# Optimization experiments

Measured on AMD Instinct MI355X. Metric: run time of the kernel, lower is better.

Reference implementation:

```python
import jax, jax.numpy as jnp
import numpy as np
import math

D_MODEL = 512
N_HEADS = 8
D_HEAD = D_MODEL // N_HEADS
B, T = 2, 2048


def quant_linear(x, W, b, bitwidth):
    # BitNet-b1.58 style: ternary weights (per-tensor absmean scale),
    # activations quantized to signed `bitwidth` with per-token absmax scale.
    ws = jnp.mean(jnp.abs(W)) + 1e-5
    Wq = jnp.clip(jnp.round(W / ws), -1.0, 1.0)
    Qb = 2.0 ** (bitwidth - 1) - 1.0
    xs = Qb / (jnp.max(jnp.abs(x), axis=-1, keepdims=True) + 1e-5)
    xq = jnp.clip(jnp.round(x * xs), -Qb, Qb)
    return (xq @ W.T if False else jnp.einsum('...i,oi->...o', xq, Wq)) * (ws / xs) + b


def layer_norm(x, g, b, eps=1e-5):
    mu = jnp.mean(x, axis=-1, keepdims=True)
    var = jnp.mean(jnp.square(x - mu), axis=-1, keepdims=True)
    return (x - mu) * jax.lax.rsqrt(var + eps) * g + b


def rel_shift(x):
    # x: [B, H, T, T]
    b, h, t1, t2 = x.shape
    x = jnp.pad(x, ((0, 0), (0, 0), (0, 0), (1, 0)))  # [B,H,T,T+1]
    x = x.reshape(b, h, t2 + 1, t1)[:, :, 1:, :]
    return x.reshape(b, h, t1, t2)


def setup_inputs() -> dict:
    key = jax.random.key(0)
    ks = jax.random.split(key, 16)
    s = 0.02
    inp = {
        'x': jax.random.normal(ks[0], (B, T, D_MODEL), jnp.float32),
        'mask': jnp.ones((B, T, T), jnp.int32),
        'pos_emb': jax.random.normal(ks[1], (1, T, D_MODEL), jnp.float32),
        'ln_g': jnp.ones((D_MODEL,), jnp.float32),
        'ln_b': jnp.zeros((D_MODEL,), jnp.float32),
        'Wq': jax.random.normal(ks[2], (D_MODEL, D_MODEL), jnp.float32) * s,
        'bq': jnp.zeros((D_MODEL,), jnp.float32),
        'Wk': jax.random.normal(ks[3], (D_MODEL, D_MODEL), jnp.float32) * s,
        'bk': jnp.zeros((D_MODEL,), jnp.float32),
        'Wv': jax.random.normal(ks[4], (D_MODEL, D_MODEL), jnp.float32) * s,
        'bv': jnp.zeros((D_MODEL,), jnp.float32),
        'Wp': jax.random.normal(ks[5], (D_MODEL, D_MODEL), jnp.float32) * s,
        'bp': jnp.zeros((D_MODEL,), jnp.float32),
        'Wo': jax.random.normal(ks[6], (D_MODEL, D_MODEL), jnp.float32) * s,
        'bo': jnp.zeros((D_MODEL,), jnp.float32),
        'pos_bias_u': jax.random.normal(ks[7], (N_HEADS, D_HEAD), jnp.float32) * 0.01,
        'pos_bias_v': jax.random.normal(ks[8], (N_HEADS, D_HEAD), jnp.float32) * 0.01,
        'bitwidth': 8,
    }
    return inp


def reference(x, mask, pos_emb, ln_g, ln_b, Wq, bq, Wk, bk, Wv, bv, Wp, bp, Wo, bo, pos_bias_u, pos_bias_v, bitwidth):
    b, t, c = x.shape
    y = layer_norm(x, ln_g, ln_b)
    # projections -> [B, H, T, Dh]
    Q = quant_linear(y, Wq, bq, bitwidth).reshape(b, t, N_HEADS, D_HEAD).transpose(0, 2, 1, 3)
    K = quant_linear(y, Wk, bk, bitwidth).reshape(b, t, N_HEADS, D_HEAD).transpose(0, 2, 1, 3)
    V = quant_linear(y, Wv, bv, bitwidth).reshape(b, t, N_HEADS, D_HEAD).transpose(0, 2, 1, 3)
    p = quant_linear(pos_emb, Wp, bp, bitwidth).reshape(1, t, N_HEADS, D_HEAD).transpose(0, 2, 1, 3)
    Qu = Q + pos_bias_u[None, :, None, :]
    Qv = Q + pos_bias_v[None, :, None, :]
    matrix_ac = jnp.einsum('bhqd,bhkd->bhqk', Qu, K)
    matrix_bd = rel_shift(jnp.einsum('bhqd,xhkd->bhqk', Qv, p))
    scores = (matrix_ac + matrix_bd) / math.sqrt(D_HEAD)
    scores = jnp.where(mask[:, None, :, :] == 0, -jnp.inf, scores)
    A = jnp.nan_to_num(jax.nn.softmax(scores, axis=-1), nan=0.0)
    H = jnp.einsum('bhqk,bhkd->bhqd', A, V).transpose(0, 2, 1, 3).reshape(b, t, c)
    H = quant_linear(H, Wo, bo, bitwidth)
    H = H * mask[:, :, 0:1].astype(H.dtype)  # seq mask
    return x + H
```

## Files before the change

kernel.cpp:

```cpp
#include <hip/hip_runtime.h>
#include <math.h>

#define TT 2048
#define DMODEL 512
#define NHEADS 8
#define DHEAD 64
#define NBATCH 2
#define MTOK (NBATCH*TT)
#define NSPLIT 4
#define SC 0.18033688011112042f
#define PADQ 68

typedef unsigned short u16;
typedef unsigned int u32;
typedef __bf16 bf16x8 __attribute__((ext_vector_type(8)));
typedef float f32x4 __attribute__((ext_vector_type(4)));
typedef short s16x4 __attribute__((ext_vector_type(4)));
typedef short s16x8 __attribute__((ext_vector_type(8)));
typedef unsigned short u16x4 __attribute__((ext_vector_type(4)));
typedef int s32x4 __attribute__((ext_vector_type(4)));

#define MFMA16(a,b,c) __builtin_amdgcn_mfma_f32_16x16x32_bf16(a,b,c,0,0,0)
#define MFMA_PV(a,b,c) __builtin_amdgcn_mfma_f32_16x16x16bf16_1k(a,b,c,0,0,0)

__device__ __forceinline__ u16 f2b(float f){
  u32 x = __float_as_uint(f);
  x = x + 0x7fffu + ((x >> 16) & 1u);
  return (u16)(x >> 16);
}
__device__ __forceinline__ float b2f(u16 u){
  return __uint_as_float(((u32)u) << 16);
}
__device__ __forceinline__ u32 cvtpk(float lo, float hi){
  u32 d; asm("v_cvt_pk_bf16_f32 %0, %1, %2" : "=v"(d) : "v"(lo), "v"(hi)); return d;
}
__device__ __forceinline__ size_t fidx(int t, int d){
  return ((size_t)((t>>4)*16 + (d>>5)))*512
       + (size_t)(((((d>>3)&3)*16) + (t&15))*8 + (d&7));
}

__global__ __launch_bounds__(256) void wprep1_kernel(
    const float* __restrict__ W0, const float* __restrict__ W1,
    const float* __restrict__ W2, const float* __restrict__ W3,
    const float* __restrict__ W4, float* __restrict__ partial)
{
  int widx = blockIdx.y;
  const float* W = (widx==0)?W0:(widx==1)?W1:(widx==2)?W2:(widx==3)?W3:W4;
  size_t base = (size_t)blockIdx.x * 4096;
  int tid = threadIdx.x;
  float s = 0.f;
  for (int i = tid; i < 4096; i += 256) s += fabsf(W[base + i]);
  __shared__ float red[256];
  red[tid] = s; __syncthreads();
  for (int o = 128; o > 0; o >>= 1){ if (tid < o) red[tid] += red[tid+o]; __syncthreads(); }
  if (tid == 0) partial[widx*64 + blockIdx.x] = red[0];
}

__global__ __launch_bounds__(256) void wprep2_kernel(
    const float* __restrict__ W0, const float* __restrict__ W1,
    const float* __restrict__ W2, const float* __restrict__ W3,
    const float* __restrict__ W4, const float* __restrict__ partial,
    float* __restrict__ wsv, u16* __restrict__ wt)
{
  int widx = blockIdx.y;
  const float* W = (widx==0)?W0:(widx==1)?W1:(widx==2)?W2:(widx==3)?W3:W4;
  __shared__ float red[64];
  int tid = threadIdx.x;
  if (tid < 64) red[tid] = partial[widx*64 + tid];
  __syncthreads();
  for (int o = 32; o > 0; o >>= 1){ if (tid < o) red[tid] += red[tid+o]; __syncthreads(); }
  float ws = red[0] * (1.0f/262144.0f) + 1e-5f;
  if (blockIdx.x == 0 && tid == 0) wsv[widx] = ws;
  int base = blockIdx.x * 1024;
  for (int i = tid; i < 1024; i += 256){
    int idx = base + i;
    int n = idx >> 9, k = idx & 511;
    float v = rintf(W[idx] / ws);
    v = fminf(fmaxf(v, -1.f), 1.f);
    wt[(size_t)widx*262144 + fidx(n, k)] = f2b(v);
  }
}

__global__ __launch_bounds__(256) void lnq_kernel(
    const float* __restrict__ x, const float* __restrict__ g, const float* __restrict__ b,
    const int* __restrict__ bwp, u16* __restrict__ xq, float* __restrict__ stok)
{
  int t = blockIdx.x;
  const float* xr = x + (size_t)t * DMODEL;
  int tid = threadIdx.x;
  float v0 = xr[tid], v1 = xr[tid + 256];
  __shared__ float red[256];
  red[tid] = v0 + v1; __syncthreads();
  for (int o=128;o>0;o>>=1){ if(tid<o) red[tid]+=red[tid+o]; __syncthreads(); }
  float mu = red[0] * (1.0f/512.0f);
  __syncthreads();
  float d0 = v0 - mu, d1 = v1 - mu;
  red[tid] = d0*d0 + d1*d1; __syncthreads();
  for (int o=128;o>0;o>>=1){ if(tid<o) red[tid]+=red[tid+o]; __syncthreads(); }
  float var = red[0] * (1.0f/512.0f);
  __syncthreads();
  float rs = rsqrtf(var + 1e-5f);
  float y0 = d0*rs*g[tid] + b[tid];
  float y1 = d1*rs*g[tid+256] + b[tid+256];
  red[tid] = fmaxf(fabsf(y0), fabsf(y1)); __syncthreads();
  for (int o=128;o>0;o>>=1){ if(tid<o) red[tid]=fmaxf(red[tid],red[tid+o]); __syncthreads(); }
  float amax = red[0];
  float Qb = (float)((1 << (bwp[0]-1)) - 1);
  float xs = Qb / (amax + 1e-5f);
  if (tid == 0) stok[t] = (amax + 1e-5f) / Qb;
  float q0 = fminf(fmaxf(rintf(y0 * xs), -Qb), Qb);
  float q1 = fminf(fmaxf(rintf(y1 * xs), -Qb), Qb);
  xq[fidx(t, tid)]       = f2b(q0);
  xq[fidx(t, tid + 256)] = f2b(q1);
}

__global__ __launch_bounds__(256) void quant_kernel(
    const float* __restrict__ src, const int* __restrict__ bwp,
    u16* __restrict__ xq, float* __restrict__ stok)
{
  int t = blockIdx.x;
  const float* xr = src + (size_t)t * DMODEL;
  int tid = threadIdx.x;
  float v0 = xr[tid], v1 = xr[tid + 256];
  __shared__ float red[256];
  red[tid] = fmaxf(fabsf(v0), fabsf(v1)); __syncthreads();
  for (int o=128;o>0;o>>=1){ if(tid<o) red[tid]=fmaxf(red[tid],red[tid+o]); __syncthreads(); }
  float amax = red[0];
  float Qb = (float)((1 << (bwp[0]-1)) - 1);
  float xs = Qb / (amax + 1e-5f);
  if (tid == 0) stok[t] = (amax + 1e-5f) / Qb;
  float q0 = fminf(fmaxf(rintf(v0 * xs), -Qb), Qb);
  float q1 = fminf(fmaxf(rintf(v1 * xs), -Qb), Qb);
  xq[fidx(t, tid)]       = f2b(q0);
  xq[fidx(t, tid + 256)] = f2b(q1);
}

__global__ __launch_bounds__(256) void maskflag_kernel(const int* __restrict__ mask, int* __restrict__ rowflag){
  int row = blockIdx.x;
  int tid = threadIdx.x;
  int ok = 1;
  const int* mr = mask + (size_t)row * TT;
  for (int i = tid; i < TT; i += 256) ok &= (mr[i] != 0);
  __shared__ int red[256];
  red[tid] = ok; __syncthreads();
  for (int o=128;o>0;o>>=1){ if(tid<o) red[tid] &= red[tid+o]; __syncthreads(); }
  if (tid == 0) rowflag[row] = red[0];
}

__global__ __launch_bounds__(256) void qkvgemm_kernel(
    const u16* __restrict__ Af, const u16* __restrict__ wtf,
    const float* __restrict__ stok, const float* __restrict__ wsv,
    const float* __restrict__ bq, const float* __restrict__ bk, const float* __restrict__ bv,
    const float* __restrict__ pbu, const float* __restrict__ pbv,
    u16* __restrict__ Qu, u16* __restrict__ Qv, u16* __restrict__ Kf, u16* __restrict__ Vf)
{
  int w = threadIdx.x >> 6, lane = threadIdx.x & 63;
  int g = lane >> 4, li = lane & 15;
  int mb = blockIdx.y*64 + w*16;
  int nb = blockIdx.x*64;
  int widx = nb >> 9;
  int ntb = (nb & 511) >> 4;
  f32x4 acc[4] = {{0,0,0,0},{0,0,0,0},{0,0,0,0},{0,0,0,0}};
  const u16* Ab = Af + (size_t)(mb >> 4)*16*512 + lane*8;
  const u16* Bb = wtf + (size_t)widx*262144 + (size_t)ntb*16*512 + lane*8;
  for (int kb = 0; kb < 16; kb++){
    bf16x8 a = *(const bf16x8*)(Ab + kb*512);
#pragma unroll
    for (int f = 0; f < 4; f++){
      bf16x8 bb = *(const bf16x8*)(Bb + (f*16 + kb)*512);
      acc[f] = MFMA16(a, bb, acc[f]);
    }
  }
  float ws = wsv[widx];
  const float* bias = (widx==0)?bq:(widx==1)?bk:bv;
  float sc[4];
#pragma unroll
  for (int r=0;r<4;r++) sc[r] = ws * stok[mb + 4*g + r];
#pragma unroll
  for (int f=0;f<4;f++){
    int n = nb + 16*f + li;
    int nq = n & 511;
    float bn = bias[nq];
#pragma unroll
    for (int r=0;r<4;r++){
      int m = mb + 4*g + r;
      float val = acc[f][r]*sc[r] + bn;
      int bb_ = m >> 11, t = m & (TT-1); int h = nq >> 6, d = nq & 63;
      int bh = bb_*NHEADS + h;
      if (widx == 0){
        size_t o = (((size_t)bh)*TT + t)*DHEAD + d;
        Qu[o] = f2b((val + pbu[nq])*SC);
        Qv[o] = f2b(val + pbv[nq]);
      } else if (widx == 1){
        size_t o = (((size_t)bh*128 + (t>>4))*2 + (d>>5))*512
                 + (size_t)((((d>>3)&3)*16 + (t&15))*8 + (d&7));
        Kf[o] = f2b(val);
      } else {
        size_t o = (((size_t)bh*128 + (t>>4))*2 + (d>>5))*512
                 + (size_t)(((((t>>2)&3)*16) + (d&15))*8 + (((d>>4)&1)*4) + (t&3));
        Vf[o] = f2b(val);
      }
    }
  }
}

template<int NF>
__global__ __launch_bounds__(256) void qgemm_kernel(
    const u16* __restrict__ Af, const u16* __restrict__ Wtf,
    const float* __restrict__ stok, const float* __restrict__ wsv, int widx,
    const float* __restrict__ bias, int mode,
    u16* __restrict__ outA, float* __restrict__ outF,
    const float* __restrict__ xin, const int* __restrict__ mask)
{
  int w = threadIdx.x >> 6, lane = threadIdx.x & 63;
  int g = lane >> 4, li = lane & 15;
  int mb = blockIdx.y*64 + w*16;
  int nb = blockIdx.x*(16*NF);
  f32x4 acc[NF];
#pragma unroll
  for (int f=0; f<NF; f++) acc[f] = (f32x4){0,0,0,0};
  const u16* Ab = Af + (size_t)(mb >> 4)*16*512 + lane*8;
  const u16* Bb = Wtf + (size_t)(nb >> 4)*16*512 + lane*8;
  for (int kb = 0; kb < 16; kb++){
    bf16x8 a = *(const bf16x8*)(Ab + kb*512);
#pragma unroll
    for (int f = 0; f < NF; f++){
      bf16x8 bb = *(const bf16x8*)(Bb + (f*16 + kb)*512);
      acc[f] = MFMA16(a, bb, acc[f]);
    }
  }
  float ws = wsv[widx];
  float sc[4];
#pragma unroll
  for (int r=0;r<4;r++) sc[r] = ws * stok[mb + 4*g + r];
#pragma unroll
  for (int f=0;f<NF;f++){
    int n = nb + 16*f + li;
    float bn = bias[n];
#pragma unroll
    for (int r=0;r<4;r++){
      int m = mb + 4*g + r;
      float val = acc[f][r]*sc[r] + bn;
      if (mode == 3){
        int h = n >> 6, d = n & 63;
        size_t o = (((size_t)h*128 + (m>>4))*2 + (d>>5))*512
                 + (size_t)((((d>>3)&3)*16 + (m&15))*8 + (d&7));
        outA[o] = f2b(val);
      } else {
        int bb_ = m >> 11, t = m & (TT-1);
        float mv = (float)mask[((size_t)bb_*TT + t)*TT];
        outF[(size_t)m*DMODEL + n] = xin[(size_t)m*DMODEL + n] + val*mv;
      }
    }
  }
}

__global__ __launch_bounds__(256) void bd_kernel(
    const u16* __restrict__ Qv, const u16* __restrict__ Pf, u16* __restrict__ bdsw)
{
  __shared__ u16 lds[64*PADQ];
  int tid = threadIdx.x;
  int w = tid >> 6, lane = tid & 63;
  int g = lane >> 4, li = lane & 15;
  int bh = blockIdx.z, h = bh & 7;
  int qb = blockIdx.y*64, k0 = blockIdx.x*64;
  int qt = qb + 16*w;
  {
    u32* l32 = (u32*)lds;
    for (int i = tid; i < 64*PADQ/2; i += 256) l32[i] = 0;
  }
  __syncthreads();
  const u16* Pbh = Pf + (size_t)h*128*1024;
  const u16* Qbh = Qv + (size_t)bh*TT*DHEAD;
  int qp = 16*w + 4*g;
  {
    const u16* qr = Qbh + (size_t)(qt + li)*DHEAD;
    bf16x8 a0 = *(const bf16x8*)(qr + 8*g);
    bf16x8 a1 = *(const bf16x8*)(qr + 32 + 8*g);
    int dkq = k0 - qt;
    for (int i = 0; i < 5; i++){
      if (dkq + 16*i > 15) break;
      int jt = k0 + TT - 16 - qt + 16*i;
      int j = jt + li;
      bool jok = (j <= TT-1);
      int jc = jok ? j : (TT-1);
      const u16* pr = Pbh + (size_t)(jc>>4)*1024 + (size_t)((g*16 + (jc&15))*8);
      f32x4 c = {0,0,0,0};
      c = MFMA16(a0, *(const bf16x8*)(pr),       c);
      c = MFMA16(a1, *(const bf16x8*)(pr + 512), c);
      int kp = 16*i - 15 + li + 4*g;
#pragma unroll
      for (int r = 0; r < 4; r++){
        int kpr = kp + r;
        if (jok && kpr >= 0 && kpr < 64)
          lds[kpr*PADQ + qp + r] = f2b(c[r]*SC);
      }
    }
  }
  {
    int q2r = qt + 1 + li; if (q2r > TT-1) q2r = TT-1;
    const u16* qr = Qbh + (size_t)q2r*DHEAD;
    bf16x8 a0 = *(const bf16x8*)(qr + 8*g);
    bf16x8 a1 = *(const bf16x8*)(qr + 32 + 8*g);
    int dqk = qt - k0;
    for (int i = 5; i >= 0; i--){
      if (16*i < dqk + 17) break;
      int jt2 = k0 - qt - 32 + 16*i;
      int j2 = jt2 + li;
      bool jok = (j2 >= 0);
      int jc = jok ? j2 : 0;
      const u16* pr = Pbh + (size_t)(jc>>4)*1024 + (size_t)((g*16 + (jc&15))*8);
      f32x4 c = {0,0,0,0};
      c = MFMA16(a0, *(const bf16x8*)(pr),       c);
      c = MFMA16(a1, *(const bf16x8*)(pr + 512), c);
      int kp = 16*i - 30 + li + 4*g;
#pragma unroll
      for (int r = 0; r < 4; r++){
        int kpr = kp + r;
        if (jok && kpr >= 0 && kpr < 64)
          lds[kpr*PADQ + qp + r] = f2b(c[r]*SC);
      }
    }
  }
  __syncthreads();
  {
    int kq = tid >> 4, qg = tid & 15;
    u16 vals[4][4];
#pragma unroll
    for (int kk = 0; kk < 4; kk++){
      u16x4 v = *(const u16x4*)(&lds[(4*kq + kk)*PADQ + 4*qg]);
#pragma unroll
      for (int qq = 0; qq < 4; qq++) vals[kk][qq] = v[qq];
    }
    u16* ob = bdsw + (size_t)bh*TT*TT + ((size_t)((k0>>2) + kq)*TT + qb + 4*qg)*4;
#pragma unroll
    for (int qq = 0; qq < 4; qq++){
      u16x4 o;
#pragma unroll
      for (int kk = 0; kk < 4; kk++) o[kk] = vals[kk][qq];
      *(u16x4*)(ob + qq*4) = o;
    }
  }
}

__global__ __launch_bounds__(256) void flash_kernel(
    const u16* __restrict__ Qu, const u16* __restrict__ Kf,
    const u16* __restrict__ Vf, const u16* __restrict__ bdsw,
    const int* __restrict__ mask, const int* __restrict__ rowflag,
    u16* __restrict__ Opart, float* __restrict__ Mpart, float* __restrict__ Lpart)
{
  int w = threadIdx.x >> 6, lane = threadIdx.x & 63;
  int g = lane >> 4, li = lane & 15;
  int bh = blockIdx.y; int b = bh >> 3, h = bh & 7;
  int z = blockIdx.z;
  int qb = blockIdx.x*64 + w*16;
  int q = qb + li;

  const u16* qrow = Qu + ((size_t)bh*TT + q)*DHEAD;
  bf16x8 qu0 = *(const bf16x8*)(qrow + 8*g);
  bf16x8 qu1 = *(const bf16x8*)(qrow + 32 + 8*g);

  f32x4 acc[4] = {{0,0,0,0},{0,0,0,0},{0,0,0,0},{0,0,0,0}};
  float mrun = -3e38f, lrun = 0.f;
  int rf = rowflag[b*TT + q];
  bool needmask = (__all(rf) == 0);

  const u16* kfb = Kf + (size_t)bh*128*1024;
  const u16* vfb = Vf + (size_t)bh*128*1024;
  const u16* bdb = bdsw + (size_t)bh*TT*TT;
  const int* maskq = mask + ((size_t)b*TT + q)*TT;

  int kbeg = z * (TT/NSPLIT);
  for (int k0 = kbeg; k0 < kbeg + TT/NSPLIT; k0 += 64){
    int kb = k0 >> 4;
    f32x4 s[4];
#pragma unroll
    for (int kc = 0; kc < 4; kc++){
      const u16* kp = kfb + (size_t)(kb + kc)*1024 + lane*8;
      f32x4 t_ = {0,0,0,0};
      t_ = MFMA16(*(const bf16x8*)(kp),       qu0, t_);
      t_ = MFMA16(*(const bf16x8*)(kp + 512), qu1, t_);
      s[kc] = t_;
    }
#pragma unroll
    for (int kc = 0; kc < 4; kc++){
      u16x4 bd4 = *(const u16x4*)(bdb + ((size_t)((k0>>2) + 4*kc + g)*TT + q)*4);
#pragma unroll
      for (int r = 0; r < 4; r++) s[kc][r] += b2f(bd4[r]);
    }
    if (needmask && !rf){
#pragma unroll
      for (int kc = 0; kc < 4; kc++){
        s32x4 mv = *(const s32x4*)(maskq + k0 + 16*kc + 4*g);
#pragma unroll
        for (int r = 0; r < 4; r++)
          if (mv[r] == 0) s[kc][r] = -3e38f;
      }
    }
    float tm = s[0][0];
#pragma unroll
    for (int kc = 0; kc < 4; kc++)
#pragma unroll
      for (int r = 0; r < 4; r++) tm = fmaxf(tm, s[kc][r]);
    tm = fmaxf(tm, __shfl_xor(tm, 16));
    tm = fmaxf(tm, __shfl_xor(tm, 32));
    float mn;
    if (__all(tm <= mrun)){
      mn = mrun;
    } else {
      mn = fmaxf(mrun, tm);
      float fscq = __builtin_amdgcn_exp2f(mrun - mn);
      mrun = mn;
      lrun *= fscq;
#pragma unroll
      for (int r = 0; r < 4; r++){
        float fr = __shfl(fscq, 4*g + r);
        acc[0][r] *= fr; acc[1][r] *= fr; acc[2][r] *= fr; acc[3][r] *= fr;
      }
    }
    float ps = 0.f;
    s16x4 pk[4];
#pragma unroll
    for (int kc = 0; kc < 4; kc++){
      float p0 = __builtin_amdgcn_exp2f(s[kc][0] - mn);
      float p1 = __builtin_amdgcn_exp2f(s[kc][1] - mn);
      float p2 = __builtin_amdgcn_exp2f(s[kc][2] - mn);
      float p3 = __builtin_amdgcn_exp2f(s[kc][3] - mn);
      ps += (p0 + p1) + (p2 + p3);
      union { u32 w[2]; s16x4 v; } u_;
      u_.w[0] = cvtpk(p0, p1);
      u_.w[1] = cvtpk(p2, p3);
      pk[kc] = u_.v;
    }
    ps += __shfl_xor(ps, 16);
    ps += __shfl_xor(ps, 32);
    lrun += ps;
#pragma unroll
    for (int kc = 0; kc < 4; kc++){
      const u16* vp = vfb + (size_t)(kb + kc)*1024 + lane*8;
      bf16x8 v0 = *(const bf16x8*)(vp);
      bf16x8 v1 = *(const bf16x8*)(vp + 512);
      s16x8 w0 = (s16x8)v0, w1 = (s16x8)v1;
      acc[0] = MFMA_PV(pk[kc], __builtin_shufflevector(w0, w0, 0,1,2,3), acc[0]);
      acc[1] = MFMA_PV(pk[kc], __builtin_shufflevector(w0, w0, 4,5,6,7), acc[1]);
      acc[2] = MFMA_PV(pk[kc], __builtin_shufflevector(w1, w1, 0,1,2,3), acc[2]);
      acc[3] = MFMA_PV(pk[kc], __builtin_shufflevector(w1, w1, 4,5,6,7), acc[3]);
    }
  }
#pragma unroll
  for (int r = 0; r < 4; r++){
    size_t o = ((size_t)(b*TT + qb + 4*g + r)*NSPLIT + z)*DMODEL + h*DHEAD + li;
    Opart[o]      = f2b(acc[0][r]);
    Opart[o + 16] = f2b(acc[1][r]);
    Opart[o + 32] = f2b(acc[2][r]);
    Opart[o + 48] = f2b(acc[3][r]);
  }
  if (lane < 16){
    size_t mo = ((size_t)(b*TT + qb + li)*NSPLIT + z)*NHEADS + h;
    Mpart[mo] = mrun;
    Lpart[mo] = lrun;
  }
}

__global__ __launch_bounds__(256) void merge_kernel(
    const u16* __restrict__ Opart, const float* __restrict__ Mpart, const float* __restrict__ Lpart,
    const int* __restrict__ bwp, u16* __restrict__ xq, float* __restrict__ stok)
{
  int tok = blockIdx.x, tid = threadIdx.x;
  __shared__ float scl[NSPLIT][NHEADS];
  if (tid < NHEADS){
    int h = tid;
    float ms[NSPLIT], ls[NSPLIT];
#pragma unroll
    for (int s = 0; s < NSPLIT; s++){
      ms[s] = Mpart[((size_t)tok*NSPLIT + s)*NHEADS + h];
      ls[s] = Lpart[((size_t)tok*NSPLIT + s)*NHEADS + h];
    }
    float mst = ms[0];
#pragma unroll
    for (int s = 1; s < NSPLIT; s++) mst = fmaxf(mst, ms[s]);
    float sc_[NSPLIT]; float lst = 0.f;
#pragma unroll
    for (int s = 0; s < NSPLIT; s++){
      sc_[s] = __builtin_amdgcn_exp2f(ms[s] - mst);
      lst += ls[s]*sc_[s];
    }
    float inv = (lst > 0.f) ? 1.0f/lst : 0.f;
#pragma unroll
    for (int s = 0; s < NSPLIT; s++) scl[s][h] = sc_[s]*inv;
  }
  __syncthreads();
  float hv[2];
#pragma unroll
  for (int j = 0; j < 2; j++){
    int idx = tid + 256*j;
    int h = idx >> 6;
    float a = 0.f;
#pragma unroll
    for (int s = 0; s < NSPLIT; s++)
      a += b2f(Opart[((size_t)tok*NSPLIT + s)*DMODEL + idx]) * scl[s][h];
    hv[j] = a;
  }
  __shared__ float red[256];
  red[tid] = fmaxf(fabsf(hv[0]), fabsf(hv[1])); __syncthreads();
  for (int o=128;o>0;o>>=1){ if(tid<o) red[tid]=fmaxf(red[tid],red[tid+o]); __syncthreads(); }
  float amax = red[0];
  float Qb = (float)((1 << (bwp[0]-1)) - 1);
  float xs = Qb / (amax + 1e-5f);
  if (tid == 0) stok[tok] = (amax + 1e-5f) / Qb;
#pragma unroll
  for (int j = 0; j < 2; j++){
    int idx = tid + 256*j;
    float qv = fminf(fmaxf(rintf(hv[j] * xs), -Qb), Qb);
    xq[fidx(tok, idx)] = f2b(qv);
  }
}

extern "C" void kernel_launch(void* const* d_in, const int* in_sizes, int n_in,
                              void* d_out, int out_size, void* d_ws, size_t ws_size,
                              hipStream_t stream) {
  const float* x    = (const float*)d_in[0];
  const int*   mask = (const int*)  d_in[1];
  const float* pos  = (const float*)d_in[2];
  const float* lng  = (const float*)d_in[3];
  const float* lnb  = (const float*)d_in[4];
  const float* Wq   = (const float*)d_in[5];
  const float* bq   = (const float*)d_in[6];
  const float* Wk   = (const float*)d_in[7];
  const float* bk   = (const float*)d_in[8];
  const float* Wv   = (const float*)d_in[9];
  const float* bv   = (const float*)d_in[10];
  const float* Wp   = (const float*)d_in[11];
  const float* bp   = (const float*)d_in[12];
  const float* Wo   = (const float*)d_in[13];
  const float* bo   = (const float*)d_in[14];
  const float* pbu  = (const float*)d_in[15];
  const float* pbv  = (const float*)d_in[16];
  const int*   bwp  = (const int*)  d_in[17];
  float* out = (float*)d_out;

  char* wsb = (char*)d_ws;
  size_t off = 0;
  auto alloc = [&](size_t nbytes)->char* {
    char* p = wsb + off;
    off = (off + nbytes + 255) & ~(size_t)255;
    return p;
  };
  float* partial = (float*)alloc(5*64*sizeof(float));
  float* wsv     = (float*)alloc(5*sizeof(float));
  u16*   wt      = (u16*)  alloc((size_t)5*262144*2);
  float* stok_y  = (float*)alloc(MTOK*sizeof(float));
  float* stok_p  = (float*)alloc(TT*sizeof(float));
  u16*   Qu      = (u16*)  alloc((size_t)16*TT*DHEAD*2);
  u16*   Qv      = (u16*)  alloc((size_t)16*TT*DHEAD*2);
  u16*   Kf      = (u16*)  alloc((size_t)16*TT*DHEAD*2);
  u16*   Vf      = (u16*)  alloc((size_t)16*TT*DHEAD*2);
  u16*   pool    = (u16*)  alloc((size_t)MTOK*NSPLIT*DMODEL*2);
  u16*   xq_y    = pool;
  u16*   xq_p    = pool + (size_t)MTOK*DMODEL;
  u16*   Pf      = xq_p + (size_t)TT*DMODEL;
  u16*   Opart   = pool;
  float* Mpart   = (float*)alloc((size_t)MTOK*NSPLIT*NHEADS*sizeof(float));
  float* Lpart   = (float*)alloc((size_t)MTOK*NSPLIT*NHEADS*sizeof(float));
  u16*   xq_H    = (u16*)  alloc((size_t)MTOK*DMODEL*2);
  float* stok_H  = (float*)alloc(MTOK*sizeof(float));
  int*   rowflag = (int*)  alloc(MTOK*sizeof(int));
  u16*   bds     = (u16*)  alloc((size_t)16*TT*TT*2);
  if (off > ws_size) return;

  wprep1_kernel<<<dim3(64,5), 256, 0, stream>>>(Wq, Wk, Wv, Wp, Wo, partial);
  wprep2_kernel<<<dim3(256,5), 256, 0, stream>>>(Wq, Wk, Wv, Wp, Wo, partial, wsv, wt);
  lnq_kernel<<<MTOK, 256, 0, stream>>>(x, lng, lnb, bwp, xq_y, stok_y);
  quant_kernel<<<TT, 256, 0, stream>>>(pos, bwp, xq_p, stok_p);
  maskflag_kernel<<<MTOK, 256, 0, stream>>>(mask, rowflag);
  qkvgemm_kernel<<<dim3(24,64), 256, 0, stream>>>(xq_y, wt, stok_y, wsv, bq, bk, bv, pbu, pbv,
                                                  Qu, Qv, Kf, Vf);
  qgemm_kernel<2><<<dim3(16,32), 256, 0, stream>>>(xq_p, wt + (size_t)3*262144, stok_p, wsv, 3, bp, 3,
                                                   Pf, nullptr, nullptr, nullptr);
  bd_kernel<<<dim3(32,32,16), 256, 0, stream>>>(Qv, Pf, bds);
  flash_kernel<<<dim3(32,16,NSPLIT), 256, 0, stream>>>(Qu, Kf, Vf, bds, mask, rowflag,
                                                       Opart, Mpart, Lpart);
  merge_kernel<<<MTOK, 256, 0, stream>>>(Opart, Mpart, Lpart, bwp, xq_H, stok_H);
  qgemm_kernel<2><<<dim3(16,64), 256, 0, stream>>>(xq_H, wt + (size_t)4*262144, stok_H, wsv, 4, bo, 4,
                                                   nullptr, out, x, mask);
}
```

Baseline: 196.0 us.

## Fuse relative-position BD scores into flash attention, dropping the BD buffer

Removes the separate bd_kernel, which wrote a 16×T×T bf16 rel-shifted position-score matrix to global memory that flash_kernel then read back. Flash attention now computes the shifted Qv·P scores per key tile with extra MFMAs and stages them in a per-wave LDS row before adding them to the content scores. This trades a large global write and read for extra matrix work and LDS traffic inside the attention loop. Pf gets its own allocation so it no longer aliases the pool that Opart overwrites.

```diff
diff --git a/kernel.cpp b/kernel.cpp
--- a/kernel.cpp
+++ b/kernel.cpp
@@ -9,7 +9,6 @@
 #define MTOK (NBATCH*TT)
 #define NSPLIT 4
 #define SC 0.18033688011112042f
-#define PADQ 68
 
 typedef unsigned short u16;
 typedef unsigned int u32;
@@ -255,110 +254,34 @@
   }
 }
 
-__global__ __launch_bounds__(256) void bd_kernel(
-    const u16* __restrict__ Qv, const u16* __restrict__ Pf, u16* __restrict__ bdsw)
-{
-  __shared__ u16 lds[64*PADQ];
-  int tid = threadIdx.x;
-  int w = tid >> 6, lane = tid & 63;
-  int g = lane >> 4, li = lane & 15;
-  int bh = blockIdx.z, h = bh & 7;
-  int qb = blockIdx.y*64, k0 = blockIdx.x*64;
-  int qt = qb + 16*w;
-  {
-    u32* l32 = (u32*)lds;
-    for (int i = tid; i < 64*PADQ/2; i += 256) l32[i] = 0;
-  }
-  __syncthreads();
-  const u16* Pbh = Pf + (size_t)h*128*1024;
-  const u16* Qbh = Qv + (size_t)bh*TT*DHEAD;
-  int qp = 16*w + 4*g;
-  {
-    const u16* qr = Qbh + (size_t)(qt + li)*DHEAD;
-    bf16x8 a0 = *(const bf16x8*)(qr + 8*g);
-    bf16x8 a1 = *(const bf16x8*)(qr + 32 + 8*g);
-    int dkq = k0 - qt;
-    for (int i = 0; i < 5; i++){
-      if (dkq + 16*i > 15) break;
-      int jt = k0 + TT - 16 - qt + 16*i;
-      int j = jt + li;
-      bool jok = (j <= TT-1);
-      int jc = jok ? j : (TT-1);
-      const u16* pr = Pbh + (size_t)(jc>>4)*1024 + (size_t)((g*16 + (jc&15))*8);
-      f32x4 c = {0,0,0,0};
-      c = MFMA16(a0, *(const bf16x8*)(pr),       c);
-      c = MFMA16(a1, *(const bf16x8*)(pr + 512), c);
-      int kp = 16*i - 15 + li + 4*g;
-#pragma unroll
-      for (int r = 0; r < 4; r++){
-        int kpr = kp + r;
-        if (jok && kpr >= 0 && kpr < 64)
-          lds[kpr*PADQ + qp + r] = f2b(c[r]*SC);
-      }
-    }
-  }
-  {
-    int q2r = qt + 1 + li; if (q2r > TT-1) q2r = TT-1;
-    const u16* qr = Qbh + (size_t)q2r*DHEAD;
-    bf16x8 a0 = *(const bf16x8*)(qr + 8*g);
-    bf16x8 a1 = *(const bf16x8*)(qr + 32 + 8*g);
-    int dqk = qt - k0;
-    for (int i = 5; i >= 0; i--){
-      if (16*i < dqk + 17) break;
-      int jt2 = k0 - qt - 32 + 16*i;
-      int j2 = jt2 + li;
-      bool jok = (j2 >= 0);
-      int jc = jok ? j2 : 0;
-      const u16* pr = Pbh + (size_t)(jc>>4)*1024 + (size_t)((g*16 + (jc&15))*8);
-      f32x4 c = {0,0,0,0};
-      c = MFMA16(a0, *(const bf16x8*)(pr),       c);
-      c = MFMA16(a1, *(const bf16x8*)(pr + 512), c);
-      int kp = 16*i - 30 + li + 4*g;
-#pragma unroll
-      for (int r = 0; r < 4; r++){
-        int kpr = kp + r;
-        if (jok && kpr >= 0 && kpr < 64)
-          lds[kpr*PADQ + qp + r] = f2b(c[r]*SC);
-      }
-    }
-  }
-  __syncthreads();
-  {
-    int kq = tid >> 4, qg = tid & 15;
-    u16 vals[4][4];
-#pragma unroll
-    for (int kk = 0; kk < 4; kk++){
-      u16x4 v = *(const u16x4*)(&lds[(4*kq + kk)*PADQ + 4*qg]);
-#pragma unroll
-      for (int qq = 0; qq < 4; qq++) vals[kk][qq] = v[qq];
-    }
-    u16* ob = bdsw + (size_t)bh*TT*TT + ((size_t)((k0>>2) + kq)*TT + qb + 4*qg)*4;
-#pragma unroll
-    for (int qq = 0; qq < 4; qq++){
-      u16x4 o;
-#pragma unroll
-      for (int kk = 0; kk < 4; kk++) o[kk] = vals[kk][qq];
-      *(u16x4*)(ob + qq*4) = o;
-    }
-  }
-}
-
 __global__ __launch_bounds__(256) void flash_kernel(
-    const u16* __restrict__ Qu, const u16* __restrict__ Kf,
-    const u16* __restrict__ Vf, const u16* __restrict__ bdsw,
+    const u16* __restrict__ Qu, const u16* __restrict__ Qv,
+    const u16* __restrict__ Kf, const u16* __restrict__ Vf,
+    const u16* __restrict__ Pf,
     const int* __restrict__ mask, const int* __restrict__ rowflag,
     u16* __restrict__ Opart, float* __restrict__ Mpart, float* __restrict__ Lpart)
 {
+  __shared__ float bdt[64][68];
   int w = threadIdx.x >> 6, lane = threadIdx.x & 63;
   int g = lane >> 4, li = lane & 15;
   int bh = blockIdx.y; int b = bh >> 3, h = bh & 7;
   int z = blockIdx.z;
-  int qb = blockIdx.x*64 + w*16;
-  int q = qb + li;
+  int qb = blockIdx.x*64;
+  int qt = qb + 16*w;
+  int q  = qt + li;
 
   const u16* qrow = Qu + ((size_t)bh*TT + q)*DHEAD;
   bf16x8 qu0 = *(const bf16x8*)(qrow + 8*g);
   bf16x8 qu1 = *(const bf16x8*)(qrow + 32 + 8*g);
+  const u16* vr0 = Qv + ((size_t)bh*TT + q)*DHEAD;
+  bf16x8 qv00 = *(const bf16x8*)(vr0 + 8*g);
+  bf16x8 qv01 = *(const bf16x8*)(vr0 + 32 + 8*g);
+  int q1 = (q < TT-1) ? (q+1) : (TT-1);
+  const u16* vr1 = Qv + ((size_t)bh*TT + q1)*DHEAD;
+  bf16x8 qv10 = *(const bf16x8*)(vr1 + 8*g);
+  bf16x8 qv11 = *(const bf16x8*)(vr1 + 32 + 8*g);
+
+  float* bdrow = &bdt[16*w + li][0];
 
   f32x4 acc[4] = {{0,0,0,0},{0,0,0,0},{0,0,0,0},{0,0,0,0}};
   float mrun = -3e38f, lrun = 0.f;
@@ -367,8 +290,11 @@
 
   const u16* kfb = Kf + (size_t)bh*128*1024;
   const u16* vfb = Vf + (size_t)bh*128*1024;
-  const u16* bdb = bdsw + (size_t)bh*TT*TT;
+  const u16* Pl  = Pf + (size_t)h*128*1024 + lane*8;
   const int* maskq = mask + ((size_t)b*TT + q)*TT;
+
+  int kofs_lo = 4*g - (2047 - qt - li);
+  int kofs_up = 4*g + qt + li + 2;
 
   int kbeg = z * (TT/NSPLIT);
   for (int k0 = kbeg; k0 < kbeg + TT/NSPLIT; k0 += 64){
@@ -382,11 +308,46 @@
       t_ = MFMA16(*(const bf16x8*)(kp + 512), qu1, t_);
       s[kc] = t_;
     }
+    {
+      int JL0 = (k0 + 2032 - qt) & ~15;
+      int jl1 = (k0 + 2110 - qt) & ~15;
+      int JL1 = (jl1 < 2032) ? jl1 : 2032;
+      for (int jt = JL0; jt <= JL1; jt += 16){
+        const u16* pp = Pl + jt*64;
+        f32x4 c = {0,0,0,0};
+        c = MFMA16(*(const bf16x8*)(pp),       qv00, c);
+        c = MFMA16(*(const bf16x8*)(pp + 512), qv01, c);
+        int kp2 = jt + kofs_lo - k0;
+#pragma unroll
+        for (int r = 0; r < 4; r++){
+          int kpr = kp2 + r;
+          if ((unsigned)kpr < 64u) bdrow[kpr] = c[r]*SC;
+        }
+      }
+      int ju0 = (k0 - qt - 17) & ~15;
+      int JU0 = (ju0 > 0) ? ju0 : 0;
+      int ju1 = (k0 + 61 - qt) & ~15;
+      int JU1 = (ju1 < 2032) ? ju1 : 2032;
+      for (int jt = JU0; jt <= JU1; jt += 16){
+        const u16* pp = Pl + jt*64;
+        f32x4 c = {0,0,0,0};
+        c = MFMA16(*(const bf16x8*)(pp),       qv10, c);
+        c = MFMA16(*(const bf16x8*)(pp + 512), qv11, c);
+        int kp2 = jt + kofs_up - k0;
+#pragma unroll
+        for (int r = 0; r < 4; r++){
+          int kpr = kp2 + r;
+          if ((unsigned)kpr < 64u) bdrow[kpr] = c[r]*SC;
+        }
+      }
+      int kd = q + 1 - k0;
+      if ((unsigned)kd < 64u) bdrow[kd] = 0.f;
+    }
 #pragma unroll
     for (int kc = 0; kc < 4; kc++){
-      u16x4 bd4 = *(const u16x4*)(bdb + ((size_t)((k0>>2) + 4*kc + g)*TT + q)*4);
-#pragma unroll
-      for (int r = 0; r < 4; r++) s[kc][r] += b2f(bd4[r]);
+      f32x4 bd4 = *(const f32x4*)(&bdrow[16*kc + 4*g]);
+#pragma unroll
+      for (int r = 0; r < 4; r++) s[kc][r] += bd4[r];
     }
     if (needmask && !rf){
 #pragma unroll
@@ -449,14 +410,14 @@
   }
 #pragma unroll
   for (int r = 0; r < 4; r++){
-    size_t o = ((size_t)(b*TT + qb + 4*g + r)*NSPLIT + z)*DMODEL + h*DHEAD + li;
+    size_t o = ((size_t)(b*TT + qb + 16*w + 4*g + r)*NSPLIT + z)*DMODEL + h*DHEAD + li;
     Opart[o]      = f2b(acc[0][r]);
     Opart[o + 16] = f2b(acc[1][r]);
     Opart[o + 32] = f2b(acc[2][r]);
     Opart[o + 48] = f2b(acc[3][r]);
   }
   if (lane < 16){
-    size_t mo = ((size_t)(b*TT + qb + li)*NSPLIT + z)*NHEADS + h;
+    size_t mo = ((size_t)(b*TT + qt + li)*NSPLIT + z)*NHEADS + h;
     Mpart[mo] = mrun;
     Lpart[mo] = lrun;
   }
@@ -555,17 +516,16 @@
   u16*   Qv      = (u16*)  alloc((size_t)16*TT*DHEAD*2);
   u16*   Kf      = (u16*)  alloc((size_t)16*TT*DHEAD*2);
   u16*   Vf      = (u16*)  alloc((size_t)16*TT*DHEAD*2);
+  u16*   Pf      = (u16*)  alloc((size_t)NHEADS*TT*DHEAD*2);
   u16*   pool    = (u16*)  alloc((size_t)MTOK*NSPLIT*DMODEL*2);
   u16*   xq_y    = pool;
   u16*   xq_p    = pool + (size_t)MTOK*DMODEL;
-  u16*   Pf      = xq_p + (size_t)TT*DMODEL;
   u16*   Opart   = pool;
   float* Mpart   = (float*)alloc((size_t)MTOK*NSPLIT*NHEADS*sizeof(float));
   float* Lpart   = (float*)alloc((size_t)MTOK*NSPLIT*NHEADS*sizeof(float));
   u16*   xq_H    = (u16*)  alloc((size_t)MTOK*DMODEL*2);
   float* stok_H  = (float*)alloc(MTOK*sizeof(float));
   int*   rowflag = (int*)  alloc(MTOK*sizeof(int));
-  u16*   bds     = (u16*)  alloc((size_t)16*TT*TT*2);
   if (off > ws_size) return;
 
   wprep1_kernel<<<dim3(64,5), 256, 0, stream>>>(Wq, Wk, Wv, Wp, Wo, partial);
@@ -577,8 +537,7 @@
                                                   Qu, Qv, Kf, Vf);
   qgemm_kernel<2><<<dim3(16,32), 256, 0, stream>>>(xq_p, wt + (size_t)3*262144, stok_p, wsv, 3, bp, 3,
                                                    Pf, nullptr, nullptr, nullptr);
-  bd_kernel<<<dim3(32,32,16), 256, 0, stream>>>(Qv, Pf, bds);
-  flash_kernel<<<dim3(32,16,NSPLIT), 256, 0, stream>>>(Qu, Kf, Vf, bds, mask, rowflag,
+  flash_kernel<<<dim3(32,16,NSPLIT), 256, 0, stream>>>(Qu, Qv, Kf, Vf, Pf, mask, rowflag,
                                                        Opart, Mpart, Lpart);
   merge_kernel<<<MTOK, 256, 0, stream>>>(Opart, Mpart, Lpart, bwp, xq_H, stok_H);
   qgemm_kernel<2><<<dim3(16,64), 256, 0, stream>>>(xq_H, wt + (size_t)4*262144, stok_H, wsv, 4, bo, 4,
```

After: 213.3 us. +8.8%, slower.
